# Performance work log

Hardware: AMD Instinct MI355X
Metric: run time of the kernel (lower is better)

Reference implementation:

```python
import jax, jax.numpy as jnp
import numpy as np
import math

DIM = 3      # coordinate dim per node
N_NODES = 15 # 45 / 3
HEADS = 3
D_K = 1


def _spatial_graph():
    # ST-GCN style 15-joint skeleton: (self, inward, outward) adjacency, shape (3,15,15)
    edges = [(1, 0), (2, 1), (3, 2), (4, 0), (5, 4), (6, 5), (7, 0),
             (8, 7), (9, 8), (10, 9), (11, 8), (12, 11), (13, 8), (14, 13)]
    self_a = np.eye(N_NODES, dtype=np.float32)
    inward = np.zeros((N_NODES, N_NODES), dtype=np.float32)
    for i, j in edges:
        inward[i, j] = 1.0
    outward = inward.T.copy()
    return jnp.asarray(np.stack([self_a, inward, outward], axis=0))


def setup_inputs() -> dict:
    key = jax.random.key(0)
    ks = jax.random.split(key, 11)
    bs, T, F = 32, 2048, DIM * N_NODES
    bound3 = 1.0 / math.sqrt(DIM)
    bound45 = 1.0 / math.sqrt(F)
    return {
        "q": jax.random.normal(ks[0], (bs, T, F), jnp.float32),
        "k": jax.random.normal(ks[1], (bs, T, F), jnp.float32),
        "v": jax.random.normal(ks[2], (bs, T, F), jnp.float32),
        "wq": jax.random.uniform(ks[3], (DIM, DIM), jnp.float32, -bound3, bound3),
        "bq": jax.random.uniform(ks[4], (DIM,), jnp.float32, -bound3, bound3),
        "wk": jax.random.uniform(ks[5], (DIM, DIM), jnp.float32, -bound3, bound3),
        "bk": jax.random.uniform(ks[6], (DIM,), jnp.float32, -bound3, bound3),
        "wv": jax.random.uniform(ks[7], (DIM, DIM), jnp.float32, -bound3, bound3),
        "bv": jax.random.uniform(ks[8], (DIM,), jnp.float32, -bound3, bound3),
        "wo": jax.random.uniform(ks[9], (F, F), jnp.float32, -bound45, bound45),
        "bo": jax.random.uniform(ks[10], (F,), jnp.float32, -bound45, bound45),
        "graph": _spatial_graph(),
        "is_test": 0,
    }


def _project(x, w, b, bs, T):
    # (bs,T,45) -> (bs,T,3,15) -> (bs,T,15,3) -> linear -> (bs,T,15,3,1) -> (bs,T,3,15,1)
    x = x.reshape(bs, T, DIM, N_NODES).transpose(0, 1, 3, 2)
    x = x @ w.T + b
    return x.reshape(bs, T, N_NODES, HEADS, D_K).transpose(0, 1, 3, 2, 4)


def reference(q, k, v, wq, bq, wk, bk, wv, bv, wo, bo, graph, is_test):
    bs, T, F = q.shape
    qh = _project(q, wq, bq, bs, T)  # (bs,T,h,15,1)
    kh = _project(k, wk, bk, bs, T)
    vh = _project(v, wv, bv, bs, T)
    # abs scores with graph mask, shape (bs,T,h,15,15)
    scores = jnp.abs(jnp.einsum('bthnd,bthmd->bthnm', qh, kh) / math.sqrt(D_K))
    graph_tot = graph.sum(0)  # (15,15)
    scores = jnp.where(graph_tot == 0, jnp.float32(-1e9), scores)
    # softmax over flattened 15*15 grid
    att = jax.nn.softmax(scores.reshape(bs, T, HEADS, N_NODES * N_NODES), axis=-1)
    att = att.reshape(bs, T, HEADS, N_NODES, N_NODES)
    out = jnp.einsum('bthnm,bthmd->bthnd', att, vh)  # (bs,T,h,15,1)
    concat = out.transpose(0, 1, 3, 2, 4).reshape(bs, T, F)
    return concat @ wo.T + bo
```

## Files before the change

kernel.cpp:

```cpp
#include <hip/hip_runtime.h>


#define SLAB 2880

__device__ __forceinline__ void glds16(const float* g, float* l) {
  __builtin_amdgcn_global_load_lds(
      (const __attribute__((address_space(1))) void*)g,
      (__attribute__((address_space(3))) void*)l, 16, 0, 0);
}

__global__ void __launch_bounds__(192, 3)
mha_spatial_kernel(const float* __restrict__ q, const float* __restrict__ k,
                   const float* __restrict__ v,
                   const float* __restrict__ wq, const float* __restrict__ bq,
                   const float* __restrict__ wk, const float* __restrict__ bk,
                   const float* __restrict__ wv, const float* __restrict__ bv,
                   const float* __restrict__ wo, const float* __restrict__ bo,
                   float* __restrict__ out)
{
  constexpr int PN[43] = {0,1,2,3,4,5,6,7,8,9,10,11,12,13,14,
                          1,0, 2,1, 3,2, 4,0, 5,4, 6,5, 7,0,
                          8,7, 9,8, 10,9, 11,8, 12,11, 13,8, 14,13};
  constexpr int PM[43] = {0,1,2,3,4,5,6,7,8,9,10,11,12,13,14,
                          0,1, 1,2, 2,3, 0,4, 4,5, 5,6, 0,7,
                          7,8, 8,9, 9,10, 8,11, 11,12, 8,13, 13,14};

  __shared__ float sm[3 * SLAB];
  const int tid = threadIdx.x;
  const int p = tid & 63;
  const int h = tid >> 6;
  const int hu = __builtin_amdgcn_readfirstlane(h);
  const size_t base = (size_t)blockIdx.x * SLAB;

  {
    const float* gq = q + base;
    const float* gk = k + base;
    const float* gv = v + base;
    float* l0 = sm;
    float* l1 = sm + SLAB;
    float* l2 = sm + 2 * SLAB;
#pragma unroll
    for (int i = 0; i < 4; ++i) {
      const int idx = i * 192 + tid;
      if (idx < 720) {
        const int off = idx * 4;
        glds16(gq + off, l0 + off);
        glds16(gk + off, l1 + off);
        glds16(gv + off, l2 + off);
      }
    }
  }

  const float wq0 = wq[hu*3+0], wq1 = wq[hu*3+1], wq2 = wq[hu*3+2], bq0 = bq[hu];
  const float wk0 = wk[hu*3+0], wk1 = wk[hu*3+1], wk2 = wk[hu*3+2], bk0 = bk[hu];
  const float wv0 = wv[hu*3+0], wv1 = wv[hu*3+1], wv2 = wv[hu*3+2], bv0 = bv[hu];

  __syncthreads();

  const float* xq = sm + p * 45;
  const float* xk = sm + SLAB + p * 45;
  const float* xv = sm + 2 * SLAB + p * 45;

  float aq[15], ak[15], vv[15];
#pragma unroll
  for (int n = 0; n < 15; ++n) {
    aq[n] = fabsf(bq0 + xq[n] * wq0 + xq[15 + n] * wq1 + xq[30 + n] * wq2);
    ak[n] = fabsf(bk0 + xk[n] * wk0 + xk[15 + n] * wk1 + xk[30 + n] * wk2);
    vv[n] = bv0 + xv[n] * wv0 + xv[15 + n] * wv1 + xv[30 + n] * wv2;
  }
  float mx = 0.0f;
#pragma unroll
  for (int i = 0; i < 43; ++i) mx = fmaxf(mx, aq[PN[i]] * ak[PM[i]]);
  float Z = 0.0f;
  float oh[15];
#pragma unroll
  for (int n = 0; n < 15; ++n) oh[n] = 0.0f;
#pragma unroll
  for (int i = 0; i < 43; ++i) {
    const float e = __expf(aq[PN[i]] * ak[PM[i]] - mx);
    Z += e;
    oh[PN[i]] += e * vv[PM[i]];
  }
  const float rz = 1.0f / Z;

  __syncthreads();

  {
    float* crow = sm + p * 45;
#pragma unroll
    for (int n = 0; n < 15; ++n) crow[n * 3 + hu] = oh[n] * rz;
  }
  __syncthreads();

  {
    float cg[45];
    const float* crow = sm + p * 45;
#pragma unroll
    for (int g = 0; g < 45; ++g) cg[g] = crow[g];
    float acc[15];
#pragma unroll
    for (int j = 0; j < 15; ++j) acc[j] = bo[hu * 15 + j];
#pragma unroll
    for (int g = 0; g < 45; ++g) {
#pragma unroll
      for (int j = 0; j < 15; ++j)
        acc[j] = fmaf(cg[g], wo[(hu * 15 + j) * 45 + g], acc[j]);
    }
    float* yrow = sm + SLAB + p * 45;
#pragma unroll
    for (int j = 0; j < 15; ++j) yrow[hu * 15 + j] = acc[j];
  }
  __syncthreads();

  float* gout = out + base;
  const float* ysrc = sm + SLAB;
#pragma unroll
  for (int i = 0; i < 4; ++i) {
    const int idx = i * 192 + tid;
    if (idx < 720)
      *(float4*)(gout + idx * 4) = *(const float4*)(ysrc + idx * 4);
  }
}

extern "C" void kernel_launch(void* const* d_in, const int* in_sizes, int n_in,
                              void* d_out, int out_size, void* d_ws, size_t ws_size,
                              hipStream_t stream) {
  const float* q  = (const float*)d_in[0];
  const float* k  = (const float*)d_in[1];
  const float* v  = (const float*)d_in[2];
  const float* wq = (const float*)d_in[3];
  const float* bq = (const float*)d_in[4];
  const float* wk = (const float*)d_in[5];
  const float* bk = (const float*)d_in[6];
  const float* wv = (const float*)d_in[7];
  const float* bv = (const float*)d_in[8];
  const float* wo = (const float*)d_in[9];
  const float* bo = (const float*)d_in[10];
  float* out = (float*)d_out;

  hipLaunchKernelGGL(mha_spatial_kernel, dim3(1024), dim3(192), 0, stream,
                     q, k, v, wq, bq, wk, bk, wv, bv, wo, bo, out);
}
```

Baseline: 18.08 us.

## Double block size, split output projection across two wave groups, cheaper softmax max

Launches 384 threads per block, with two wave groups per head that each redundantly compute attention and then split the 45x45 output projection in half, roughly 8 of the head's 15 output columns each. The softmax max is now bounded by max(|q|)*max(|k|) instead of a 43-term scan, and the Z sum is split into two accumulators to shorten the dependency chain. This cuts per-thread FMA work in the projection, which dominates, and raises wave parallelism per block. The cost is duplicated projection and softmax work and a launch bound of 6 blocks that may not fit in registers.

```diff
diff --git a/kernel.cpp b/kernel.cpp
--- a/kernel.cpp
+++ b/kernel.cpp
@@ -9,7 +9,17 @@
       (__attribute__((address_space(3))) void*)l, 16, 0, 0);
 }
 
-__global__ void __launch_bounds__(192, 3)
+__device__ __forceinline__ float tmax15(const float* a) {
+  float m01 = fmaxf(a[0], a[1]), m23 = fmaxf(a[2], a[3]);
+  float m45 = fmaxf(a[4], a[5]), m67 = fmaxf(a[6], a[7]);
+  float m89 = fmaxf(a[8], a[9]), mab = fmaxf(a[10], a[11]);
+  float mcd = fmaxf(a[12], a[13]);
+  float x0 = fmaxf(m01, m23), x1 = fmaxf(m45, m67);
+  float x2 = fmaxf(m89, mab), x3 = fmaxf(mcd, a[14]);
+  return fmaxf(fmaxf(x0, x1), fmaxf(x2, x3));
+}
+
+__global__ void __launch_bounds__(384, 6)
 mha_spatial_kernel(const float* __restrict__ q, const float* __restrict__ k,
                    const float* __restrict__ v,
                    const float* __restrict__ wq, const float* __restrict__ bq,
@@ -28,8 +38,11 @@
   __shared__ float sm[3 * SLAB];
   const int tid = threadIdx.x;
   const int p = tid & 63;
-  const int h = tid >> 6;
+  const int w = tid >> 6;
+  const int h = (w >= 3) ? (w - 3) : w;
+  const int s = (w >= 3) ? 1 : 0;
   const int hu = __builtin_amdgcn_readfirstlane(h);
+  const int su = __builtin_amdgcn_readfirstlane(s);
   const size_t base = (size_t)blockIdx.x * SLAB;
 
   {
@@ -40,8 +53,8 @@
     float* l1 = sm + SLAB;
     float* l2 = sm + 2 * SLAB;
 #pragma unroll
-    for (int i = 0; i < 4; ++i) {
-      const int idx = i * 192 + tid;
+    for (int i = 0; i < 2; ++i) {
+      const int idx = i * 384 + tid;
       if (idx < 720) {
         const int off = idx * 4;
         glds16(gq + off, l0 + off);
@@ -68,55 +81,64 @@
     ak[n] = fabsf(bk0 + xk[n] * wk0 + xk[15 + n] * wk1 + xk[30 + n] * wk2);
     vv[n] = bv0 + xv[n] * wv0 + xv[15 + n] * wv1 + xv[30 + n] * wv2;
   }
-  float mx = 0.0f;
-#pragma unroll
-  for (int i = 0; i < 43; ++i) mx = fmaxf(mx, aq[PN[i]] * ak[PM[i]]);
-  float Z = 0.0f;
+  const float mx = tmax15(aq) * tmax15(ak);
+  float Z0 = 0.0f, Z1 = 0.0f;
   float oh[15];
 #pragma unroll
   for (int n = 0; n < 15; ++n) oh[n] = 0.0f;
 #pragma unroll
   for (int i = 0; i < 43; ++i) {
     const float e = __expf(aq[PN[i]] * ak[PM[i]] - mx);
-    Z += e;
+    if (i & 1) Z1 += e; else Z0 += e;
     oh[PN[i]] += e * vv[PM[i]];
   }
-  const float rz = 1.0f / Z;
+  const float rz = 1.0f / (Z0 + Z1);
 
   __syncthreads();
 
   {
     float* crow = sm + p * 45;
 #pragma unroll
-    for (int n = 0; n < 15; ++n) crow[n * 3 + hu] = oh[n] * rz;
+    for (int n = 0; n < 15; ++n) {
+      const bool mine = su ? (n >= 8) : (n < 8);
+      if (mine) crow[n * 3 + hu] = oh[n] * rz;
+    }
   }
   __syncthreads();
 
   {
+    const int fbase = hu * 15 + su * 8;
+    const int nj = su ? 7 : 8;
     float cg[45];
     const float* crow = sm + p * 45;
 #pragma unroll
     for (int g = 0; g < 45; ++g) cg[g] = crow[g];
-    float acc[15];
+    float acc[8];
 #pragma unroll
-    for (int j = 0; j < 15; ++j) acc[j] = bo[hu * 15 + j];
+    for (int j = 0; j < 8; ++j) {
+      const int f = (fbase + j < 45) ? (fbase + j) : 44;
+      acc[j] = bo[f];
+    }
 #pragma unroll
     for (int g = 0; g < 45; ++g) {
 #pragma unroll
-      for (int j = 0; j < 15; ++j)
-        acc[j] = fmaf(cg[g], wo[(hu * 15 + j) * 45 + g], acc[j]);
+      for (int j = 0; j < 8; ++j) {
+        const int f = (fbase + j < 45) ? (fbase + j) : 44;
+        acc[j] = fmaf(cg[g], wo[f * 45 + g], acc[j]);
+      }
     }
     float* yrow = sm + SLAB + p * 45;
 #pragma unroll
-    for (int j = 0; j < 15; ++j) yrow[hu * 15 + j] = acc[j];
+    for (int j = 0; j < 8; ++j)
+      if (j < nj) yrow[fbase + j] = acc[j];
   }
   __syncthreads();
 
   float* gout = out + base;
   const float* ysrc = sm + SLAB;
 #pragma unroll
-  for (int i = 0; i < 4; ++i) {
-    const int idx = i * 192 + tid;
+  for (int i = 0; i < 2; ++i) {
+    const int idx = i * 384 + tid;
     if (idx < 720)
       *(float4*)(gout + idx * 4) = *(const float4*)(ysrc + idx * 4);
   }
@@ -138,6 +160,6 @@
   const float* bo = (const float*)d_in[10];
   float* out = (float*)d_out;
 
-  hipLaunchKernelGGL(mha_spatial_kernel, dim3(1024), dim3(192), 0, stream,
+  hipLaunchKernelGGL(mha_spatial_kernel, dim3(1024), dim3(384), 0, stream,
                      q, k, v, wq, bq, wk, bk, wv, bv, wo, bo, out);
 }
```

After: 29.12 us. 1.61x slower.
